# Kernel optimization log

Hardware: AMD Instinct MI355X
Metric: run time of the kernel (lower is better)

Reference implementation:

```python
import jax, jax.numpy as jnp
import numpy as np

N_NODES = 50000
N_EDGES = 800000
IN_DIM = 128
HID = 128
N_GRAPHS = 256
N_CLASSES = 2
ALPHA = 0.2  # leaky relu slope
EPS_BN = 1e-5


def setup_inputs() -> dict:
    key = jax.random.key(0)
    ks = jax.random.split(key, 24)
    adjacency = jax.random.randint(ks[0], (2, N_EDGES), 0, N_NODES, dtype=jnp.int32)
    input_feature = jax.random.normal(ks[1], (N_NODES, IN_DIM), dtype=jnp.float32)
    graph_indicator = jnp.sort(jax.random.randint(ks[2], (N_NODES,), 0, N_GRAPHS, dtype=jnp.int32))
    labels = jax.random.randint(ks[3], (N_GRAPHS,), 0, N_CLASSES, dtype=jnp.int64)
    s = 0.05
    params = {
        'W1': jax.random.normal(ks[4], (IN_DIM, HID), jnp.float32) * s,
        'a1': jax.random.normal(ks[5], (2 * HID,), jnp.float32) * s,
        'bn2_g': jnp.ones((HID,), jnp.float32),
        'bn2_b': jnp.zeros((HID,), jnp.float32),
        'W2': jax.random.normal(ks[6], (HID, HID), jnp.float32) * s,
        'a2': jax.random.normal(ks[7], (2 * HID,), jnp.float32) * s,
        'bn3_g': jnp.ones((HID,), jnp.float32),
        'bn3_b': jnp.zeros((HID,), jnp.float32),
        'W3': jax.random.normal(ks[8], (HID, HID), jnp.float32) * s,
        'a3': jax.random.normal(ks[9], (2 * HID,), jnp.float32) * s,
        'fc1_w': jax.random.normal(ks[10], (HID, 2 * HID), jnp.float32) * s,
        'fc1_b': jnp.zeros((2 * HID,), jnp.float32),
        'fc2_w': jax.random.normal(ks[11], (2 * HID, HID), jnp.float32) * s,
        'fc2_b': jnp.zeros((HID,), jnp.float32),
        'fc3_w': jax.random.normal(ks[12], (HID, N_CLASSES), jnp.float32) * s,
        'fc3_b': jnp.zeros((N_CLASSES,), jnp.float32),
    }
    return dict(adjacency=adjacency, input_feature=input_feature,
                graph_indicator=graph_indicator, labels=labels, **params)


def _batchnorm(x, g, b):
    # training-mode BatchNorm1d over node dim (biased variance)
    mu = jnp.mean(x, axis=0)
    var = jnp.mean((x - mu) ** 2, axis=0)
    return (x - mu) * jax.lax.rsqrt(var + EPS_BN) * g + b


def _sp_gat(x, src, dst, W, a):
    # pyGAT SpGraphAttentionLayer (dropout disabled / eval mode)
    h = x @ W                                # [N, F]
    F = h.shape[1]
    e_src = h @ a[:F]                        # [N]
    e_dst = h @ a[F:]                        # [N]
    e = e_src[src] + e_dst[dst]              # [E]
    ee = jnp.exp(-jax.nn.leaky_relu(e, ALPHA))
    rowsum = jax.ops.segment_sum(ee, src, num_segments=N_NODES)          # [N]
    num = jax.ops.segment_sum(ee[:, None] * h[dst], src, num_segments=N_NODES)  # [N, F]
    h_prime = num / (rowsum[:, None] + 1e-16)
    return jax.nn.elu(h_prime)


def reference(adjacency, input_feature, graph_indicator, labels,
              W1, a1, bn2_g, bn2_b, W2, a2, bn3_g, bn3_b, W3, a3,
              fc1_w, fc1_b, fc2_w, fc2_b, fc3_w, fc3_b):
    src, dst = adjacency[0], adjacency[1]
    # bn1 output is discarded in the original forward
    x = _sp_gat(input_feature, src, dst, W1, a1)
    x = _batchnorm(x, bn2_g, bn2_b)
    x = _sp_gat(x, src, dst, W2, a2)
    x = _batchnorm(x, bn3_g, bn3_b)
    x = _sp_gat(x, src, dst, W3, a3)
    # pooling_sum_4tensor: per-graph sum pooling
    pooled = jax.ops.segment_sum(x, graph_indicator, num_segments=N_GRAPHS)  # [G, F]
    x = jax.nn.relu(pooled @ fc1_w + fc1_b)
    x = jax.nn.relu(x @ fc2_w + fc2_b)
    logits = x @ fc3_w + fc3_b
    return logits
```

## Files before the change

kernel.cpp:

```cpp
#include <hip/hip_runtime.h>
#include <hip/hip_bf16.h>

#define N_NODES 50000
#define N_EDGES 800000
#define FD 128
#define N_GRAPHS 256
#define NPART 6250

typedef unsigned short u16;
typedef short bf16x8 __attribute__((ext_vector_type(8)));
typedef float f32x4 __attribute__((ext_vector_type(4)));

__device__ __forceinline__ u16 f2bf(float v) {
    __hip_bfloat16 h = __float2bfloat16(v);
    union { __hip_bfloat16 hh; u16 u; } c; c.hh = h; return c.u;
}
__device__ __forceinline__ float bf2f(u16 r) {
    return __uint_as_float(((unsigned int)r) << 16);
}

__global__ __launch_bounds__(256) void count_deg_part_k(const int* __restrict__ src,
                                                        int* __restrict__ cnt, int E) {
    int part = blockIdx.x & 7;
    int lo = part * NPART, hi = lo + NPART;
    int stride = (gridDim.x >> 3) * 256;
    for (int e = (blockIdx.x >> 3) * 256 + threadIdx.x; e < E; e += stride) {
        int s = src[e];
        if (s >= lo && s < hi) atomicAdd(&cnt[s], 1);
    }
}

__global__ __launch_bounds__(256) void fill_csr_part_k(const int* __restrict__ src,
                                                       const int* __restrict__ dst,
                                                       int* __restrict__ cur,
                                                       int* __restrict__ edst, int E) {
    int part = blockIdx.x & 7;
    int lo = part * NPART, hi = lo + NPART;
    int stride = (gridDim.x >> 3) * 256;
    for (int e = (blockIdx.x >> 3) * 256 + threadIdx.x; e < E; e += stride) {
        int s = src[e];
        if (s >= lo && s < hi) {
            int p = atomicAdd(&cur[s], 1);
            edst[p] = dst[e];
        }
    }
}

__global__ __launch_bounds__(256) void scan1_k(const int* __restrict__ cnt,
                                               int* __restrict__ bsum, int M,
                                               float* __restrict__ bnbuf,
                                               float* __restrict__ pooled) {
    int i = blockIdx.x * 256 + threadIdx.x;
    int v = (i < M) ? cnt[i] : 0;
    __shared__ int l[256];
    l[threadIdx.x] = v;
    __syncthreads();
    for (int s = 128; s > 0; s >>= 1) {
        if (threadIdx.x < s) l[threadIdx.x] += l[threadIdx.x + s];
        __syncthreads();
    }
    if (threadIdx.x == 0) bsum[blockIdx.x] = l[0];
    if (blockIdx.x == 0) {
        bnbuf[threadIdx.x] = 0.f; bnbuf[threadIdx.x + 256] = 0.f;
        for (int k = threadIdx.x; k < N_GRAPHS * FD; k += 256) pooled[k] = 0.f;
    }
}

__global__ __launch_bounds__(256) void scan3_k(const int* __restrict__ cnt,
                                               const int* __restrict__ bsum,
                                               int* __restrict__ offs,
                                               int* __restrict__ cur, int M, int NB) {
    int i = blockIdx.x * 256 + threadIdx.x;
    int tid = threadIdx.x;
    __shared__ int bs[256];
    bs[tid] = (tid < NB) ? bsum[tid] : 0;
    __syncthreads();
    for (int off = 1; off < 256; off <<= 1) {
        int t = (tid >= off) ? bs[tid - off] : 0;
        __syncthreads();
        bs[tid] += t;
        __syncthreads();
    }
    int base = (blockIdx.x == 0) ? 0 : bs[blockIdx.x - 1];
    int v = (i < M) ? cnt[i] : 0;
    __shared__ int l[256];
    l[tid] = v;
    __syncthreads();
    for (int off = 1; off < 256; off <<= 1) {
        int t = (tid >= off) ? l[tid - off] : 0;
        __syncthreads();
        l[tid] += t;
        __syncthreads();
    }
    int excl = l[tid] - v + base;
    if (i < M) { offs[i] = excl; cur[i] = excl; }
    if (i == M - 1) offs[M] = excl + v;
}

__global__ __launch_bounds__(256) void gemm_mfma_k(const float* __restrict__ Xf,
                                                   const u16* __restrict__ Xb,
                                                   int use_f32,
                                                   const float* __restrict__ W,
                                                   const float* __restrict__ sums,
                                                   const float* __restrict__ sumsq,
                                                   const float* __restrict__ g,
                                                   const float* __restrict__ b,
                                                   float invN, int haveBN,
                                                   const float* __restrict__ avec,
                                                   u16* __restrict__ Hb,
                                                   float* __restrict__ es,
                                                   float* __restrict__ ed, int M) {
    __shared__ u16 As[64][136];
    __shared__ u16 Bs[128][136];
    __shared__ float cv[128];
    __shared__ float scsh[256];
    int tid = threadIdx.x;
    int row0 = blockIdx.x * 64;

    if (haveBN) {
        if (tid < 128) {
            float mu = sums[tid] * invN;
            float var = sumsq[tid] * invN - mu * mu;
            float sc = g[tid] * rsqrtf(var + 1e-5f);
            scsh[tid] = sc;
            scsh[128 + tid] = b[tid] - mu * sc;
        }
        __syncthreads();
        float cvp = 0.f;
#pragma unroll 8
        for (int i = 0; i < 64; i++) {
            int idx = i * 256 + tid;
            int k = idx >> 7;
            int n = idx & 127;
            float wv = W[idx];
            Bs[n][k] = f2bf(scsh[k] * wv);
            cvp += scsh[128 + k] * wv;
        }
        __syncthreads();
        scsh[tid] = cvp;
        __syncthreads();
        if (tid < 128) cv[tid] = scsh[tid] + scsh[tid + 128];
    } else {
#pragma unroll 8
        for (int i = 0; i < 64; i++) {
            int idx = i * 256 + tid;
            Bs[idx & 127][idx >> 7] = f2bf(W[idx]);
        }
        if (tid < 128) cv[tid] = 0.f;
    }

    {
        int r = tid >> 2, k0 = (tid & 3) * 32;
        int grow = row0 + r;
        if (grow < M) {
            if (use_f32) {
                const float4* s = (const float4*)(Xf + (size_t)grow * FD + k0);
#pragma unroll
                for (int u = 0; u < 8; u++) {
                    float4 v = s[u];
                    ushort4 o;
                    o.x = f2bf(v.x); o.y = f2bf(v.y); o.z = f2bf(v.z); o.w = f2bf(v.w);
                    *(ushort4*)&As[r][k0 + u * 4] = o;
                }
            } else {
                const uint4* s = (const uint4*)(Xb + (size_t)grow * FD + k0);
#pragma unroll
                for (int u = 0; u < 4; u++) *(uint4*)&As[r][k0 + u * 8] = s[u];
            }
        } else {
            uint4 z = make_uint4(0, 0, 0, 0);
#pragma unroll
            for (int u = 0; u < 4; u++) *(uint4*)&As[r][k0 + u * 8] = z;
        }
    }
    __syncthreads();

    int wave = tid >> 6, lane = tid & 63;
    int quad = lane >> 4, n16 = lane & 15;
    int rbase = wave * 16;
    f32x4 acc[8];
    f32x4 zz = {0.f, 0.f, 0.f, 0.f};
#pragma unroll
    for (int t = 0; t < 8; t++) acc[t] = zz;

#pragma unroll
    for (int kk = 0; kk < 128; kk += 32) {
        bf16x8 a = *(const bf16x8*)&As[rbase + n16][kk + quad * 8];
#pragma unroll
        for (int t = 0; t < 8; t++) {
            bf16x8 bb = *(const bf16x8*)&Bs[t * 16 + n16][kk + quad * 8];
            acc[t] = __builtin_amdgcn_mfma_f32_16x16x32_bf16(a, bb, acc[t], 0, 0, 0);
        }
    }

    float sas[8], sad[8];
#pragma unroll
    for (int t = 0; t < 8; t++) {
        sas[t] = avec[t * 16 + n16];
        sad[t] = avec[128 + t * 16 + n16];
    }

#pragma unroll
    for (int reg = 0; reg < 4; reg++) {
        int grow = row0 + rbase + quad * 4 + reg;
        float vals[8];
        float ps = 0.f, pd = 0.f;
#pragma unroll
        for (int t = 0; t < 8; t++) {
            float v = acc[t][reg] + cv[t * 16 + n16];
            vals[t] = v;
            ps += v * sas[t];
            pd += v * sad[t];
        }
#pragma unroll
        for (int o = 8; o > 0; o >>= 1) { ps += __shfl_xor(ps, o); pd += __shfl_xor(pd, o); }
        if (grow < M) {
            if (n16 == 0) { es[grow] = ps; ed[grow] = pd; }
#pragma unroll
            for (int t = 0; t < 8; t++)
                Hb[(size_t)grow * FD + t * 16 + n16] = f2bf(vals[t]);
        }
    }
}

__global__ __launch_bounds__(256) void agg_k(const u16* __restrict__ Hb,
                                             const float* __restrict__ es_,
                                             const float* __restrict__ ed_,
                                             const int* __restrict__ offs,
                                             const int* __restrict__ edst,
                                             u16* __restrict__ Out, int M) {
    int node = __builtin_amdgcn_readfirstlane((int)((blockIdx.x * blockDim.x + threadIdx.x) >> 6));
    int lane = threadIdx.x & 63;
    if (node >= M) return;
    int s0 = offs[node], s1 = offs[node + 1];
    float esv = es_[node];
    int q = lane >> 4;
    int f16 = lane & 15;
    const uint4* Hq = (const uint4*)Hb;
    float acc[8];
#pragma unroll
    for (int j = 0; j < 8; j++) acc[j] = 0.f;
    float rsl = 0.f;
    int last = s1 - 1;
    for (int e = s0; e < s1; e += 8) {
        int eA = e + q;
        int eB = e + 4 + q;
        int iA = eA <= last ? eA : last;
        int iB = eB <= last ? eB : last;
        int dA = edst[iA];
        int dB = edst[iB];
        float evA = esv + ed_[dA];
        float evB = esv + ed_[dB];
        uint4 rA = Hq[(size_t)dA * 16 + f16];
        uint4 rB = Hq[(size_t)dB * 16 + f16];
        float lrA = evA > 0.f ? evA : 0.2f * evA;
        float lrB = evB > 0.f ? evB : 0.2f * evB;
        float wA = __expf(-lrA);
        float wB = __expf(-lrB);
        if (eA > last) wA = 0.f;
        if (eB > last) wB = 0.f;
        rsl += wA + wB;
        unsigned int ra[4] = {rA.x, rA.y, rA.z, rA.w};
        unsigned int rb[4] = {rB.x, rB.y, rB.z, rB.w};
#pragma unroll
        for (int k = 0; k < 4; k++) {
            acc[2 * k]     += wA * __uint_as_float(ra[k] << 16)
                            + wB * __uint_as_float(rb[k] << 16);
            acc[2 * k + 1] += wA * __uint_as_float(ra[k] & 0xffff0000u)
                            + wB * __uint_as_float(rb[k] & 0xffff0000u);
        }
    }
    float rs = rsl;
    rs += __shfl_xor(rs, 16);
    rs += __shfl_xor(rs, 32);
#pragma unroll
    for (int j = 0; j < 8; j++) {
        acc[j] += __shfl_xor(acc[j], 16);
        acc[j] += __shfl_xor(acc[j], 32);
    }
    float inv = 1.f / (rs + 1e-16f);
    unsigned int pk[4];
#pragma unroll
    for (int k = 0; k < 4; k++) {
        float v0 = acc[2 * k] * inv;
        float v1 = acc[2 * k + 1] * inv;
        v0 = v0 > 0.f ? v0 : (__expf(v0) - 1.f);
        v1 = v1 > 0.f ? v1 : (__expf(v1) - 1.f);
        pk[k] = ((unsigned int)f2bf(v1) << 16) | f2bf(v0);
    }
    if (q == 0) {
        uint4 o = make_uint4(pk[0], pk[1], pk[2], pk[3]);
        ((uint4*)(Out + (size_t)node * FD))[f16] = o;
    }
}

__global__ void bnstats_b_k(const u16* __restrict__ Xb, float* __restrict__ sums,
                            float* __restrict__ sumsq, int M) {
    int f = threadIdx.x & 127;
    int half = threadIdx.x >> 7;
    float s1 = 0.f, s2 = 0.f;
    for (int r = blockIdx.x * 2 + half; r < M; r += gridDim.x * 2) {
        float v = bf2f(Xb[(size_t)r * FD + f]);
        s1 += v; s2 += v * v;
    }
    __shared__ float l1[256], l2[256];
    l1[threadIdx.x] = s1; l2[threadIdx.x] = s2;
    __syncthreads();
    if (half == 0) {
        atomicAdd(&sums[f], l1[f] + l1[f + 128]);
        atomicAdd(&sumsq[f], l2[f] + l2[f + 128]);
    }
}

__global__ void pool_k(const u16* __restrict__ Xb, const int* __restrict__ gi,
                       float* __restrict__ pooled, int M) {
    int f = threadIdx.x & 127;
    int half = threadIdx.x >> 7;
    int r0 = blockIdx.x * 128 + half;
    int rend = min(blockIdx.x * 128 + 128, M);
    int curg = -1; float acc = 0.f;
    for (int r = r0; r < rend; r += 2) {
        int g = gi[r];
        if (g != curg) {
            if (curg >= 0) atomicAdd(&pooled[(size_t)curg * FD + f], acc);
            curg = g; acc = 0.f;
        }
        acc += bf2f(Xb[(size_t)r * FD + f]);
    }
    if (curg >= 0) atomicAdd(&pooled[(size_t)curg * FD + f], acc);
}

__global__ __launch_bounds__(256) void mlp_k(const float* __restrict__ pooled,
                                             const float* __restrict__ fc1w, const float* __restrict__ fc1b,
                                             const float* __restrict__ fc2w, const float* __restrict__ fc2b,
                                             const float* __restrict__ fc3w, const float* __restrict__ fc3b,
                                             float* __restrict__ out) {
    int g = blockIdx.x, j = threadIdx.x;
    __shared__ float x[128], t1[256], t2[128], p0[128], p1[128];
    if (j < 128) x[j] = pooled[(size_t)g * FD + j];
    __syncthreads();
    float s = fc1b[j];
    for (int k = 0; k < 128; k++) s += x[k] * fc1w[(size_t)k * 256 + j];
    t1[j] = fmaxf(s, 0.f);
    __syncthreads();
    if (j < 128) {
        float s2 = fc2b[j];
        for (int k = 0; k < 256; k++) s2 += t1[k] * fc2w[(size_t)k * 128 + j];
        t2[j] = fmaxf(s2, 0.f);
    }
    __syncthreads();
    if (j < 128) { p0[j] = t2[j] * fc3w[j * 2]; p1[j] = t2[j] * fc3w[j * 2 + 1]; }
    __syncthreads();
    for (int s3 = 64; s3 > 0; s3 >>= 1) {
        if (j < s3) { p0[j] += p0[j + s3]; p1[j] += p1[j + s3]; }
        __syncthreads();
    }
    if (j == 0) { out[g * 2] = p0[0] + fc3b[0]; out[g * 2 + 1] = p1[0] + fc3b[1]; }
}

extern "C" void kernel_launch(void* const* d_in, const int* in_sizes, int n_in,
                              void* d_out, int out_size, void* d_ws, size_t ws_size,
                              hipStream_t stream) {
    const int*   adj  = (const int*)d_in[0];
    const float* xin  = (const float*)d_in[1];
    const int*   gi   = (const int*)d_in[2];
    const float* W1   = (const float*)d_in[4];
    const float* a1   = (const float*)d_in[5];
    const float* bn2g = (const float*)d_in[6];
    const float* bn2b = (const float*)d_in[7];
    const float* W2   = (const float*)d_in[8];
    const float* a2   = (const float*)d_in[9];
    const float* bn3g = (const float*)d_in[10];
    const float* bn3b = (const float*)d_in[11];
    const float* W3   = (const float*)d_in[12];
    const float* a3   = (const float*)d_in[13];
    const float* fc1w = (const float*)d_in[14];
    const float* fc1b = (const float*)d_in[15];
    const float* fc2w = (const float*)d_in[16];
    const float* fc2b = (const float*)d_in[17];
    const float* fc3w = (const float*)d_in[18];
    const float* fc3b = (const float*)d_in[19];
    float* out = (float*)d_out;

    const int N = N_NODES, E = N_EDGES, G = N_GRAPHS;

    u16*   Xb     = (u16*)d_ws;
    u16*   Hb     = Xb + (size_t)N * FD;
    u16*   Wt     = Hb + (size_t)N * FD;
    float* es     = (float*)(Wt + FD * FD);
    float* ed     = es + N;
    float* bnbuf  = ed + N;
    float* sumsA  = bnbuf;
    float* sumsqA = bnbuf + 128;
    float* sumsB  = bnbuf + 256;
    float* sumsqB = bnbuf + 384;
    float* cvec   = bnbuf + 512;
    float* pooled = cvec + FD;
    int*   degcnt = (int*)(pooled + (size_t)G * FD);
    int*   offs   = degcnt + N;
    int*   cur    = offs + (N + 2);
    int*   bsum   = cur + N;
    int*   edst   = bsum + 256;

    const int* srcp = adj;
    const int* dstp = adj + E;

    const int NB = (N + 255) / 256;

    hipMemsetAsync(degcnt, 0, (size_t)N * sizeof(int), stream);
    count_deg_part_k<<<8 * 392, 256, 0, stream>>>(srcp, degcnt, E);
    scan1_k<<<NB, 256, 0, stream>>>(degcnt, bsum, N, bnbuf, pooled);
    scan3_k<<<NB, 256, 0, stream>>>(degcnt, bsum, offs, cur, N, NB);
    fill_csr_part_k<<<8 * 392, 256, 0, stream>>>(srcp, dstp, cur, edst, E);

    const int gemm_grid = (N + 63) / 64;
    const int wave_grid = (N + 3) / 4;
    const float invN = 1.0f / (float)N;

    gemm_mfma_k<<<gemm_grid, 256, 0, stream>>>(xin, Xb, 1, W1,
                                               nullptr, nullptr, nullptr, nullptr, invN, 0,
                                               a1, Hb, es, ed, N);
    agg_k<<<wave_grid, 256, 0, stream>>>(Hb, es, ed, offs, edst, Xb, N);
    bnstats_b_k<<<256, 256, 0, stream>>>(Xb, sumsA, sumsqA, N);

    gemm_mfma_k<<<gemm_grid, 256, 0, stream>>>(nullptr, Xb, 0, W2,
                                               sumsA, sumsqA, bn2g, bn2b, invN, 1,
                                               a2, Hb, es, ed, N);
    agg_k<<<wave_grid, 256, 0, stream>>>(Hb, es, ed, offs, edst, Xb, N);
    bnstats_b_k<<<256, 256, 0, stream>>>(Xb, sumsB, sumsqB, N);

    gemm_mfma_k<<<gemm_grid, 256, 0, stream>>>(nullptr, Xb, 0, W3,
                                               sumsB, sumsqB, bn3g, bn3b, invN, 1,
                                               a3, Hb, es, ed, N);
    agg_k<<<wave_grid, 256, 0, stream>>>(Hb, es, ed, offs, edst, Xb, N);

    pool_k<<<(N + 127) / 128, 256, 0, stream>>>(Xb, gi, pooled, N);
    mlp_k<<<G, 256, 0, stream>>>(pooled, fc1w, fc1b, fc2w, fc2b, fc3w, fc3b, out);
}
```

Before: 420.1 us.

## Fuse CSR build and pool+MLP into cooperative grid-sync kernels

Replaces the memset, degree count, two scan kernels and CSR fill with one cooperative kernel that separates the phases with grid.sync(). Pooling and the MLP head are merged the same way. The goal is to cut launch gaps and small-kernel overhead. In exchange the CSR fill runs on only 1024 blocks instead of 3136, grid-wide barriers add their own cost, and a fallback path keeps the old launches in case the cooperative launch fails.

```diff
diff --git a/kernel.cpp b/kernel.cpp
--- a/kernel.cpp
+++ b/kernel.cpp
@@ -1,5 +1,8 @@
 #include <hip/hip_runtime.h>
 #include <hip/hip_bf16.h>
+#include <hip/hip_cooperative_groups.h>
+
+namespace cg = cooperative_groups;
 
 #define N_NODES 50000
 #define N_EDGES 800000
@@ -19,6 +22,103 @@
     return __uint_as_float(((unsigned int)r) << 16);
 }
 
+__global__ __launch_bounds__(256) void csr_coop_k(const int* __restrict__ src,
+                                                  const int* __restrict__ dst,
+                                                  int* __restrict__ cnt,
+                                                  int* __restrict__ bsum,
+                                                  int* __restrict__ offs,
+                                                  int* __restrict__ cur,
+                                                  int* __restrict__ edst,
+                                                  float* __restrict__ bnbuf,
+                                                  float* __restrict__ pooled,
+                                                  int E, int M, int NB) {
+    cg::grid_group grid = cg::this_grid();
+    int tid = threadIdx.x;
+    int bid = blockIdx.x;
+    int gsz = gridDim.x * 256;
+    int gidx = bid * 256 + tid;
+    __shared__ int l[256];
+    __shared__ int bs[256];
+
+    for (int i = gidx; i < M; i += gsz) cnt[i] = 0;
+    if (gidx < 512) bnbuf[gidx] = 0.f;
+    for (int i = gidx; i < N_GRAPHS * FD; i += gsz) pooled[i] = 0.f;
+    grid.sync();
+
+    {
+        int part = bid & 7;
+        int lo = part * NPART, hi = lo + NPART;
+        int stride = (gridDim.x >> 3) * 256;
+        for (int e = (bid >> 3) * 256 + tid; e < E; e += stride) {
+            int s = src[e];
+            if (s >= lo && s < hi) atomicAdd(&cnt[s], 1);
+        }
+    }
+    grid.sync();
+
+    for (int c = bid; c < NB; c += gridDim.x) {
+        int i = c * 256 + tid;
+        int v = (i < M) ? cnt[i] : 0;
+        l[tid] = v;
+        __syncthreads();
+        for (int s = 128; s > 0; s >>= 1) {
+            if (tid < s) l[tid] += l[tid + s];
+            __syncthreads();
+        }
+        if (tid == 0) bsum[c] = l[0];
+        __syncthreads();
+    }
+    grid.sync();
+
+    for (int c = bid; c < NB; c += gridDim.x) {
+        bs[tid] = (tid < NB) ? bsum[tid] : 0;
+        __syncthreads();
+        for (int off = 1; off < 256; off <<= 1) {
+            int t = (tid >= off) ? bs[tid - off] : 0;
+            __syncthreads();
+            bs[tid] += t;
+            __syncthreads();
+        }
+        int base = (c == 0) ? 0 : bs[c - 1];
+        int i = c * 256 + tid;
+        int v = (i < M) ? cnt[i] : 0;
+        l[tid] = v;
+        __syncthreads();
+        for (int off = 1; off < 256; off <<= 1) {
+            int t = (tid >= off) ? l[tid - off] : 0;
+            __syncthreads();
+            l[tid] += t;
+            __syncthreads();
+        }
+        int excl = l[tid] - v + base;
+        if (i < M) { offs[i] = excl; cur[i] = excl; }
+        if (i == M - 1) offs[M] = excl + v;
+        __syncthreads();
+    }
+    grid.sync();
+
+    {
+        int part = bid & 7;
+        int lo = part * NPART, hi = lo + NPART;
+        int stride = (gridDim.x >> 3) * 256;
+        for (int e = (bid >> 3) * 256 + tid; e < E; e += stride) {
+            int s = src[e];
+            if (s >= lo && s < hi) {
+                int p = atomicAdd(&cur[s], 1);
+                edst[p] = dst[e];
+            }
+        }
+    }
+}
+
+__global__ __launch_bounds__(256) void zero_k(int* __restrict__ cnt, float* __restrict__ bnbuf,
+                                              float* __restrict__ pooled, int M) {
+    int i = blockIdx.x * 256 + threadIdx.x;
+    int gsz = gridDim.x * 256;
+    for (int k = i; k < M; k += gsz) cnt[k] = 0;
+    if (i < 512) bnbuf[i] = 0.f;
+    for (int k = i; k < N_GRAPHS * FD; k += gsz) pooled[k] = 0.f;
+}
 __global__ __launch_bounds__(256) void count_deg_part_k(const int* __restrict__ src,
                                                         int* __restrict__ cnt, int E) {
     int part = blockIdx.x & 7;
@@ -29,7 +129,6 @@
         if (s >= lo && s < hi) atomicAdd(&cnt[s], 1);
     }
 }
-
 __global__ __launch_bounds__(256) void fill_csr_part_k(const int* __restrict__ src,
                                                        const int* __restrict__ dst,
                                                        int* __restrict__ cur,
@@ -45,11 +144,8 @@
         }
     }
 }
-
 __global__ __launch_bounds__(256) void scan1_k(const int* __restrict__ cnt,
-                                               int* __restrict__ bsum, int M,
-                                               float* __restrict__ bnbuf,
-                                               float* __restrict__ pooled) {
+                                               int* __restrict__ bsum, int M) {
     int i = blockIdx.x * 256 + threadIdx.x;
     int v = (i < M) ? cnt[i] : 0;
     __shared__ int l[256];
@@ -60,12 +156,7 @@
         __syncthreads();
     }
     if (threadIdx.x == 0) bsum[blockIdx.x] = l[0];
-    if (blockIdx.x == 0) {
-        bnbuf[threadIdx.x] = 0.f; bnbuf[threadIdx.x + 256] = 0.f;
-        for (int k = threadIdx.x; k < N_GRAPHS * FD; k += 256) pooled[k] = 0.f;
-    }
-}
-
+}
 __global__ __launch_bounds__(256) void scan3_k(const int* __restrict__ cnt,
                                                const int* __restrict__ bsum,
                                                int* __restrict__ offs,
@@ -312,6 +403,61 @@
     }
 }
 
+__global__ __launch_bounds__(256) void poolmlp_coop_k(const u16* __restrict__ Xb,
+                                                      const int* __restrict__ gi,
+                                                      float* __restrict__ pooled,
+                                                      const float* __restrict__ fc1w,
+                                                      const float* __restrict__ fc1b,
+                                                      const float* __restrict__ fc2w,
+                                                      const float* __restrict__ fc2b,
+                                                      const float* __restrict__ fc3w,
+                                                      const float* __restrict__ fc3b,
+                                                      float* __restrict__ out, int M) {
+    cg::grid_group grid = cg::this_grid();
+    int tid = threadIdx.x;
+    {
+        int f = tid & 127;
+        int half = tid >> 7;
+        int NC = (M + 127) / 128;
+        for (int c = blockIdx.x; c < NC; c += gridDim.x) {
+            int r0 = c * 128 + half;
+            int rend = min(c * 128 + 128, M);
+            int curg = -1; float acc = 0.f;
+            for (int r = r0; r < rend; r += 2) {
+                int g = gi[r];
+                if (g != curg) {
+                    if (curg >= 0) atomicAdd(&pooled[(size_t)curg * FD + f], acc);
+                    curg = g; acc = 0.f;
+                }
+                acc += bf2f(Xb[(size_t)r * FD + f]);
+            }
+            if (curg >= 0) atomicAdd(&pooled[(size_t)curg * FD + f], acc);
+        }
+    }
+    grid.sync();
+    int g = blockIdx.x, j = tid;
+    __shared__ float x[128], t1[256], t2[128], p0[128], p1[128];
+    if (j < 128) x[j] = pooled[(size_t)g * FD + j];
+    __syncthreads();
+    float s = fc1b[j];
+    for (int k = 0; k < 128; k++) s += x[k] * fc1w[(size_t)k * 256 + j];
+    t1[j] = fmaxf(s, 0.f);
+    __syncthreads();
+    if (j < 128) {
+        float s2 = fc2b[j];
+        for (int k = 0; k < 256; k++) s2 += t1[k] * fc2w[(size_t)k * 128 + j];
+        t2[j] = fmaxf(s2, 0.f);
+    }
+    __syncthreads();
+    if (j < 128) { p0[j] = t2[j] * fc3w[j * 2]; p1[j] = t2[j] * fc3w[j * 2 + 1]; }
+    __syncthreads();
+    for (int s3 = 64; s3 > 0; s3 >>= 1) {
+        if (j < s3) { p0[j] += p0[j + s3]; p1[j] += p1[j + s3]; }
+        __syncthreads();
+    }
+    if (j == 0) { out[g * 2] = p0[0] + fc3b[0]; out[g * 2 + 1] = p1[0] + fc3b[1]; }
+}
+
 __global__ void pool_k(const u16* __restrict__ Xb, const int* __restrict__ gi,
                        float* __restrict__ pooled, int M) {
     int f = threadIdx.x & 127;
@@ -329,7 +475,6 @@
     }
     if (curg >= 0) atomicAdd(&pooled[(size_t)curg * FD + f], acc);
 }
-
 __global__ __launch_bounds__(256) void mlp_k(const float* __restrict__ pooled,
                                              const float* __restrict__ fc1w, const float* __restrict__ fc1b,
                                              const float* __restrict__ fc2w, const float* __restrict__ fc2b,
@@ -407,11 +552,21 @@
 
     const int NB = (N + 255) / 256;
 
-    hipMemsetAsync(degcnt, 0, (size_t)N * sizeof(int), stream);
-    count_deg_part_k<<<8 * 392, 256, 0, stream>>>(srcp, degcnt, E);
-    scan1_k<<<NB, 256, 0, stream>>>(degcnt, bsum, N, bnbuf, pooled);
-    scan3_k<<<NB, 256, 0, stream>>>(degcnt, bsum, offs, cur, N, NB);
-    fill_csr_part_k<<<8 * 392, 256, 0, stream>>>(srcp, dstp, cur, edst, E);
+    {
+        int Ei = E, Ni = N, NBi = NB;
+        void* args[] = {(void*)&srcp, (void*)&dstp, (void*)&degcnt, (void*)&bsum,
+                        (void*)&offs, (void*)&cur, (void*)&edst, (void*)&bnbuf,
+                        (void*)&pooled, (void*)&Ei, (void*)&Ni, (void*)&NBi};
+        hipError_t err = hipLaunchCooperativeKernel((const void*)csr_coop_k,
+                                                    dim3(1024), dim3(256), args, 0, stream);
+        if (err != hipSuccess) {
+            zero_k<<<256, 256, 0, stream>>>(degcnt, bnbuf, pooled, N);
+            count_deg_part_k<<<8 * 392, 256, 0, stream>>>(srcp, degcnt, E);
+            scan1_k<<<NB, 256, 0, stream>>>(degcnt, bsum, N);
+            scan3_k<<<NB, 256, 0, stream>>>(degcnt, bsum, offs, cur, N, NB);
+            fill_csr_part_k<<<8 * 392, 256, 0, stream>>>(srcp, dstp, cur, edst, E);
+        }
+    }
 
     const int gemm_grid = (N + 63) / 64;
     const int wave_grid = (N + 3) / 4;
@@ -434,6 +589,16 @@
                                                a3, Hb, es, ed, N);
     agg_k<<<wave_grid, 256, 0, stream>>>(Hb, es, ed, offs, edst, Xb, N);
 
-    pool_k<<<(N + 127) / 128, 256, 0, stream>>>(Xb, gi, pooled, N);
-    mlp_k<<<G, 256, 0, stream>>>(pooled, fc1w, fc1b, fc2w, fc2b, fc3w, fc3b, out);
-}
+    {
+        int Ni = N;
+        void* args[] = {(void*)&Xb, (void*)&gi, (void*)&pooled,
+                        (void*)&fc1w, (void*)&fc1b, (void*)&fc2w, (void*)&fc2b,
+                        (void*)&fc3w, (void*)&fc3b, (void*)&out, (void*)&Ni};
+        hipError_t err = hipLaunchCooperativeKernel((const void*)poolmlp_coop_k,
+                                                    dim3(G), dim3(256), args, 0, stream);
+        if (err != hipSuccess) {
+            pool_k<<<(N + 127) / 128, 256, 0, stream>>>(Xb, gi, pooled, N);
+            mlp_k<<<G, 256, 0, stream>>>(pooled, fc1w, fc1b, fc2w, fc2b, fc3w, fc3b, out);
+        }
+    }
+}
```

Measured after the change: 860.8 us. +104.9%, slower.
